# Kernel tuning notes

Measured on AMD Instinct MI355X. Metric: run time of the kernel, lower is better.

The kernel has to match this reference:

```python
import jax, jax.numpy as jnp
import numpy as np

NUM_CLASSES = 150
FEAT_DIM = 128
N = 1_000_000
TEMPERATURE = 0.15
EPS = 1e-12


def _l2_normalize(x, axis=-1):
    # matches F.normalize(p=2): x / max(||x||, eps)
    n = jnp.sqrt(jnp.sum(x * x, axis=axis, keepdims=True))
    return x / jnp.maximum(n, EPS)


def setup_inputs() -> dict:
    key = jax.random.key(0)
    k1, k2, k3 = jax.random.split(key, 3)
    features = jax.random.normal(k1, (N, FEAT_DIM), dtype=jnp.float32)
    labels = jax.random.randint(k2, (N,), 0, NUM_CLASSES, dtype=jnp.int64)
    # prototypes buffer: random normal, L2-normalized per class (as in _initialize_prototypes)
    prototypes = _l2_normalize(jax.random.normal(k3, (NUM_CLASSES, FEAT_DIM), dtype=jnp.float32))
    return {"features": features, "labels": labels, "prototypes": prototypes}


def reference(features, labels, prototypes):
    # proto_contrastive_loss: normalize, similarity logits, per-sample CE, mean
    f = _l2_normalize(features)                      # [N, D]
    logits = (f @ prototypes.T) / TEMPERATURE        # [N, C]
    logz = jax.nn.logsumexp(logits, axis=-1)         # [N]
    picked = jnp.take_along_axis(logits, labels[:, None].astype(jnp.int32), axis=-1)[:, 0]
    losses = logz - picked                           # cross_entropy, reduction='none'
    return jnp.mean(losses)
```

## Files before the change

kernel.cpp:

```cpp
#include <hip/hip_runtime.h>


#define NS 1000000
#define NC 150
#define NCP 160
#define FD 128

static constexpr float INV_T = 1.0f / 0.15f;
static constexpr float MB = 1.0f / 0.15f;

typedef __attribute__((ext_vector_type(8))) short short8;
typedef __attribute__((ext_vector_type(4))) float f32x4;

__device__ __forceinline__ short f2bf(float x) {
    unsigned u = __builtin_bit_cast(unsigned, x);
    unsigned r = (u + 0x7fffu + ((u >> 16) & 1u)) >> 16;
    return (short)r;
}

__global__ __launch_bounds__(256) void proto_prep(
    const float* __restrict__ protos, unsigned short* __restrict__ dst)
{
    const int tid = threadIdx.x;
#pragma unroll 4
    for (int i = 0; i < (NCP * FD) / 256; ++i) {
        int idx = i * 256 + tid;
        int row = idx >> 7;
        int col = idx & 127;
        float v = (row < NC) ? protos[row * FD + col] : 0.0f;
        dst[idx] = (unsigned short)f2bf(v);
    }
}

__global__ __launch_bounds__(256) void proto_ce_mfma(
    const float*          __restrict__ feats,
    const int*            __restrict__ labels,
    const unsigned short* __restrict__ protos_bf,
    double*               __restrict__ partials)
{
    __shared__ __align__(16) char lds[NCP * FD * 2];

    const int tid = threadIdx.x;

    {
        const uint4* src = (const uint4*)protos_bf;
#pragma unroll
        for (int i = 0; i < (NCP * FD * 2) / 16 / 256; ++i) {
            int e8  = i * 256 + tid;
            int row = e8 >> 4;
            int binr = (e8 & 15) << 4;
            int dst = row * 256 + (binr ^ ((row & 7) << 4));
            *(uint4*)(lds + dst) = src[e8];
        }
    }
    __syncthreads();

    const int lane = tid & 63;
    const int wave = tid >> 6;
    const int col  = lane & 15;
    const int grp  = lane >> 4;
    const long base = ((long)blockIdx.x * 4 + wave) * 16;
    const long s    = base + col;

    float fv[32];
    const float* fp = feats + s * FD + grp * 8;
#pragma unroll
    for (int kb = 0; kb < 4; ++kb) {
        float4 a = *(const float4*)(fp + kb * 32);
        float4 b = *(const float4*)(fp + kb * 32 + 4);
        fv[kb*8+0]=a.x; fv[kb*8+1]=a.y; fv[kb*8+2]=a.z; fv[kb*8+3]=a.w;
        fv[kb*8+4]=b.x; fv[kb*8+5]=b.y; fv[kb*8+6]=b.z; fv[kb*8+7]=b.w;
    }

    float ssq = 0.0f;
#pragma unroll
    for (int i = 0; i < 32; ++i) ssq += fv[i] * fv[i];
    ssq += __shfl_xor(ssq, 16, 64);
    ssq += __shfl_xor(ssq, 32, 64);
    const float scl = rsqrtf(fmaxf(ssq, 1e-24f));

    short8 bfrag[4];
#pragma unroll
    for (int kb = 0; kb < 4; ++kb)
#pragma unroll
        for (int j = 0; j < 8; ++j)
            bfrag[kb][j] = f2bf(fv[kb*8 + j] * scl);

    f32x4 acc[10];
#pragma unroll
    for (int t = 0; t < 10; ++t) acc[t] = (f32x4){0.f, 0.f, 0.f, 0.f};

#pragma unroll
    for (int kb = 0; kb < 4; ++kb) {
#pragma unroll
        for (int t = 0; t < 10; ++t) {
            int arow  = t * 16 + col;
            int abyte = arow * 256 + ((kb * 64 + grp * 16) ^ ((arow & 7) << 4));
            short8 af = *(const short8*)(lds + abyte);
            acc[t] = __builtin_amdgcn_mfma_f32_16x16x32_bf16(af, bfrag[kb], acc[t], 0, 0, 0);
        }
    }

    const int lbl = labels[base + col];
    float ssum = 0.0f, picked = 0.0f;
#pragma unroll
    for (int t = 0; t < 10; ++t) {
#pragma unroll
        for (int r = 0; r < 4; ++r) {
            int cls = t * 16 + grp * 4 + r;
            float x = acc[t][r] * INV_T;
            float e = __expf(x - MB);
            bool valid = (cls < NC);
            ssum   += valid ? e : 0.0f;
            picked += (valid && cls == lbl) ? x : 0.0f;
        }
    }
    ssum   += __shfl_xor(ssum, 16, 64);   ssum   += __shfl_xor(ssum, 32, 64);
    picked += __shfl_xor(picked, 16, 64); picked += __shfl_xor(picked, 32, 64);

    float loss = __logf(ssum) + MB - picked;

    loss += __shfl_xor(loss, 1, 64);
    loss += __shfl_xor(loss, 2, 64);
    loss += __shfl_xor(loss, 4, 64);
    loss += __shfl_xor(loss, 8, 64);
    if (lane == 0)
        atomicAdd(&partials[blockIdx.x & 255], (double)loss);
}

__global__ __launch_bounds__(256) void proto_ce_final(
    const double* __restrict__ partials, float* __restrict__ out)
{
    const int tid = threadIdx.x;
    double v = partials[tid];
#pragma unroll
    for (int off = 32; off > 0; off >>= 1)
        v += __shfl_down(v, off, 64);
    __shared__ double w[4];
    if ((tid & 63) == 0) w[tid >> 6] = v;
    __syncthreads();
    if (tid == 0)
        out[0] = (float)((w[0] + w[1] + w[2] + w[3]) * (1.0 / (double)NS));
}

extern "C" void kernel_launch(void* const* d_in, const int* in_sizes, int n_in,
                              void* d_out, int out_size, void* d_ws, size_t ws_size,
                              hipStream_t stream)
{
    const float* feats  = (const float*)d_in[0];
    const int*   labels = (const int*)d_in[1];
    const float* protos = (const float*)d_in[2];

    unsigned short* protos_bf = (unsigned short*)d_ws;
    double* partials = (double*)((char*)d_ws + NCP * FD * 2);

    hipMemsetAsync(partials, 0, 256 * sizeof(double), stream);
    proto_prep<<<1, 256, 0, stream>>>(protos, protos_bf);
    proto_ce_mfma<<<NS / 64, 256, 0, stream>>>(feats, labels, protos_bf, partials);
    proto_ce_final<<<1, 256, 0, stream>>>(partials, (float*)d_out);
}
```

Before: 164.5 us.

## Make MFMA CE kernel persistent with prefetched feature tiles and deferred normalization

Replaces one-tile-per-wave launch with a persistent grid of 1024 blocks where each wave loops over 16-sample tiles, prefetching the next tile's features into registers while computing the current one. The prototype LDS load is amortized across many tiles and normalization scaling is folded into the exp2 argument instead of scaling each feature before bf16 conversion. This also trims the padded-class masking and label compare arithmetic. It risks lower occupancy from extra registers, and applying the scale after bf16 rounding slightly changes the rounding behaviour.

```diff
diff --git a/kernel.cpp b/kernel.cpp
--- a/kernel.cpp
+++ b/kernel.cpp
@@ -5,9 +5,14 @@
 #define NC 150
 #define NCP 160
 #define FD 128
-
-static constexpr float INV_T = 1.0f / 0.15f;
-static constexpr float MB = 1.0f / 0.15f;
+#define NTILE (NS / 16)
+#define NBLK 1024
+#define NWAVE (NBLK * 4)
+
+static constexpr float INV_T  = 1.0f / 0.15f;
+static constexpr float MB     = 1.0f / 0.15f;
+static constexpr float LOG2E  = 1.4426950408889634f;
+static constexpr float B2     = -MB * LOG2E;
 
 typedef __attribute__((ext_vector_type(8))) short short8;
 typedef __attribute__((ext_vector_type(4))) float f32x4;
@@ -32,7 +37,7 @@
     }
 }
 
-__global__ __launch_bounds__(256) void proto_ce_mfma(
+__global__ __launch_bounds__(256, 4) void proto_ce_mfma(
     const float*          __restrict__ feats,
     const int*            __restrict__ labels,
     const unsigned short* __restrict__ protos_bf,
@@ -59,73 +64,107 @@
     const int wave = tid >> 6;
     const int col  = lane & 15;
     const int grp  = lane >> 4;
-    const long base = ((long)blockIdx.x * 4 + wave) * 16;
-    const long s    = base + col;
-
-    float fv[32];
-    const float* fp = feats + s * FD + grp * 8;
-#pragma unroll
-    for (int kb = 0; kb < 4; ++kb) {
-        float4 a = *(const float4*)(fp + kb * 32);
-        float4 b = *(const float4*)(fp + kb * 32 + 4);
-        fv[kb*8+0]=a.x; fv[kb*8+1]=a.y; fv[kb*8+2]=a.z; fv[kb*8+3]=a.w;
-        fv[kb*8+4]=b.x; fv[kb*8+5]=b.y; fv[kb*8+6]=b.z; fv[kb*8+7]=b.w;
+    const int gw   = blockIdx.x * 4 + wave;
+
+    const int sw  = (col & 7) << 4;
+    const int a0  = col * 256 + ((grp * 16) ^ (sw & 0x30));
+    const int ahi = sw & 0x40;
+
+    const int lrel = -grp * 4;
+    const int vcnt = 6 - grp * 4;
+
+    float4 buf[8];
+    auto issue_loads = [&](int tile) {
+        const float4* fp = (const float4*)(feats + (long)tile * (16 * FD)) + col * (FD / 4) + grp * 2;
+#pragma unroll
+        for (int kb = 0; kb < 4; ++kb) {
+            buf[kb * 2]     = fp[kb * 8];
+            buf[kb * 2 + 1] = fp[kb * 8 + 1];
+        }
+    };
+
+    float loss_acc = 0.0f;
+    int t = gw;
+    issue_loads(t);
+
+    while (true) {
+        float ssq = 0.0f;
+#pragma unroll
+        for (int i = 0; i < 8; ++i)
+            ssq += buf[i].x * buf[i].x + buf[i].y * buf[i].y +
+                   buf[i].z * buf[i].z + buf[i].w * buf[i].w;
+        ssq += __shfl_xor(ssq, 16, 64);
+        ssq += __shfl_xor(ssq, 32, 64);
+        const float scl = rsqrtf(fmaxf(ssq, 1e-24f));
+
+        short8 bfrag[4];
+#pragma unroll
+        for (int kb = 0; kb < 4; ++kb) {
+            float4 A = buf[kb * 2], Bv = buf[kb * 2 + 1];
+            bfrag[kb][0] = f2bf(A.x);  bfrag[kb][1] = f2bf(A.y);
+            bfrag[kb][2] = f2bf(A.z);  bfrag[kb][3] = f2bf(A.w);
+            bfrag[kb][4] = f2bf(Bv.x); bfrag[kb][5] = f2bf(Bv.y);
+            bfrag[kb][6] = f2bf(Bv.z); bfrag[kb][7] = f2bf(Bv.w);
+        }
+
+        const int tn = t + NWAVE;
+        const bool more = (tn < NTILE);
+        if (more) issue_loads(tn);
+
+        const int lbl = labels[t * 16 + col];
+
+        f32x4 acc[10];
+#pragma unroll
+        for (int i = 0; i < 10; ++i) acc[i] = (f32x4){0.f, 0.f, 0.f, 0.f};
+#pragma unroll
+        for (int kb = 0; kb < 4; ++kb) {
+            const char* ap = lds + (a0 + ((kb * 64) ^ ahi));
+#pragma unroll
+            for (int tt = 0; tt < 10; ++tt) {
+                short8 af = *(const short8*)(ap + tt * 4096);
+                acc[tt] = __builtin_amdgcn_mfma_f32_16x16x32_bf16(af, bfrag[kb], acc[tt], 0, 0, 0);
+            }
+        }
+
+        const float k2 = scl * (INV_T * LOG2E);
+        const int   lm = lbl + lrel;
+        float s0 = 0.f, s1 = 0.f, s2 = 0.f, s3 = 0.f;
+        float pick = 0.0f;
+#pragma unroll
+        for (int tt = 0; tt < 10; ++tt) {
+#pragma unroll
+            for (int r = 0; r < 4; ++r) {
+                float a = acc[tt][r];
+                float e = exp2f(fmaf(a, k2, B2));
+                if (tt < 9) {
+                    if      (r == 0) s0 += e;
+                    else if (r == 1) s1 += e;
+                    else if (r == 2) s2 += e;
+                    else             s3 += e;
+                } else {
+                    s0 += (r < vcnt) ? e : 0.0f;
+                }
+                pick = (tt * 16 + r == lm) ? a : pick;
+            }
+        }
+        float ssum = (s0 + s1) + (s2 + s3);
+        ssum += __shfl_xor(ssum, 16, 64);
+        ssum += __shfl_xor(ssum, 32, 64);
+        pick += __shfl_xor(pick, 16, 64);
+        pick += __shfl_xor(pick, 32, 64);
+
+        loss_acc += __logf(ssum) + MB - pick * (scl * INV_T);
+
+        if (!more) break;
+        t = tn;
     }
 
-    float ssq = 0.0f;
-#pragma unroll
-    for (int i = 0; i < 32; ++i) ssq += fv[i] * fv[i];
-    ssq += __shfl_xor(ssq, 16, 64);
-    ssq += __shfl_xor(ssq, 32, 64);
-    const float scl = rsqrtf(fmaxf(ssq, 1e-24f));
-
-    short8 bfrag[4];
-#pragma unroll
-    for (int kb = 0; kb < 4; ++kb)
-#pragma unroll
-        for (int j = 0; j < 8; ++j)
-            bfrag[kb][j] = f2bf(fv[kb*8 + j] * scl);
-
-    f32x4 acc[10];
-#pragma unroll
-    for (int t = 0; t < 10; ++t) acc[t] = (f32x4){0.f, 0.f, 0.f, 0.f};
-
-#pragma unroll
-    for (int kb = 0; kb < 4; ++kb) {
-#pragma unroll
-        for (int t = 0; t < 10; ++t) {
-            int arow  = t * 16 + col;
-            int abyte = arow * 256 + ((kb * 64 + grp * 16) ^ ((arow & 7) << 4));
-            short8 af = *(const short8*)(lds + abyte);
-            acc[t] = __builtin_amdgcn_mfma_f32_16x16x32_bf16(af, bfrag[kb], acc[t], 0, 0, 0);
-        }
-    }
-
-    const int lbl = labels[base + col];
-    float ssum = 0.0f, picked = 0.0f;
-#pragma unroll
-    for (int t = 0; t < 10; ++t) {
-#pragma unroll
-        for (int r = 0; r < 4; ++r) {
-            int cls = t * 16 + grp * 4 + r;
-            float x = acc[t][r] * INV_T;
-            float e = __expf(x - MB);
-            bool valid = (cls < NC);
-            ssum   += valid ? e : 0.0f;
-            picked += (valid && cls == lbl) ? x : 0.0f;
-        }
-    }
-    ssum   += __shfl_xor(ssum, 16, 64);   ssum   += __shfl_xor(ssum, 32, 64);
-    picked += __shfl_xor(picked, 16, 64); picked += __shfl_xor(picked, 32, 64);
-
-    float loss = __logf(ssum) + MB - picked;
-
-    loss += __shfl_xor(loss, 1, 64);
-    loss += __shfl_xor(loss, 2, 64);
-    loss += __shfl_xor(loss, 4, 64);
-    loss += __shfl_xor(loss, 8, 64);
+    loss_acc += __shfl_xor(loss_acc, 1, 64);
+    loss_acc += __shfl_xor(loss_acc, 2, 64);
+    loss_acc += __shfl_xor(loss_acc, 4, 64);
+    loss_acc += __shfl_xor(loss_acc, 8, 64);
     if (lane == 0)
-        atomicAdd(&partials[blockIdx.x & 255], (double)loss);
+        atomicAdd(&partials[gw & 255], (double)loss_acc);
 }
 
 __global__ __launch_bounds__(256) void proto_ce_final(
@@ -154,8 +193,8 @@
     unsigned short* protos_bf = (unsigned short*)d_ws;
     double* partials = (double*)((char*)d_ws + NCP * FD * 2);
 
-    hipMemsetAsync(partials, 0, 256 * sizeof(double), stream);
+    (void)hipMemsetAsync(partials, 0, 256 * sizeof(double), stream);
     proto_prep<<<1, 256, 0, stream>>>(protos, protos_bf);
-    proto_ce_mfma<<<NS / 64, 256, 0, stream>>>(feats, labels, protos_bf, partials);
+    proto_ce_mfma<<<NBLK, 256, 0, stream>>>(feats, labels, protos_bf, partials);
     proto_ce_final<<<1, 256, 0, stream>>>(partials, (float*)d_out);
 }
```

New measurement: 471.8 us. +186.7%, slower.
